# Performance work log

Measured on AMD Instinct MI355X. Metric: run time of the kernel, lower is better.

Reference implementation:

```python
import jax, jax.numpy as jnp
import numpy as np

N_NODES = 100000
N_EDGES = 3200000
NFEAT, H1, H2, NCLASS = 512, 300, 200, 40


def setup_inputs() -> dict:
    key = jax.random.key(0)
    ks = jax.random.split(key, 8)
    x = jax.random.normal(ks[0], (N_NODES, NFEAT), dtype=jnp.float32)
    edge_index = jax.random.randint(ks[1], (2, N_EDGES), 0, N_NODES, dtype=jnp.int32)
    edge_weight = jax.random.uniform(ks[2], (N_EDGES,), dtype=jnp.float32)
    def glorot(k, fi, fo):
        s = 1.0 / np.sqrt(fi)
        return jax.random.uniform(k, (fi, fo), jnp.float32, -s, s)
    w1 = glorot(ks[3], NFEAT, H1)
    w2 = glorot(ks[4], H1, H2)
    w3 = glorot(ks[5], H2, NCLASS)
    return {
        'x': x, 'edge_index': edge_index, 'edge_weight': edge_weight,
        'w1': w1, 'b1': jnp.zeros((H1,), jnp.float32),
        'w2': w2, 'b2': jnp.zeros((H2,), jnp.float32),
        'w3': w3, 'b3': jnp.zeros((NCLASS,), jnp.float32),
    }


def _gcn_layer(h, edge_index, edge_weight, w, b):
    # support = h @ W ; out = A @ support + b  (A given as weighted edge list)
    support = h @ w                                   # [N, out]
    src, dst = edge_index[0], edge_index[1]
    msgs = support[src] * edge_weight[:, None]        # gather + scale, [E, out]
    agg = jax.ops.segment_sum(msgs, dst, num_segments=h.shape[0])
    return agg + b


def reference(x, edge_index, edge_weight, w1, b1, w2, b2, w3, b3):
    h1 = jax.nn.relu(_gcn_layer(x, edge_index, edge_weight, w1, b1))
    h2 = jax.nn.relu(_gcn_layer(h1, edge_index, edge_weight, w2, b2))
    logits = _gcn_layer(h2, edge_index, edge_weight, w3, b3)
    return jax.nn.softmax(logits, axis=1)
```

## Files before the change

### kernel.cpp

```cpp
#include <hip/hip_runtime.h>
#include <hip/hip_bf16.h>
#include <hip/hip_fp16.h>
#include <math.h>

#define NFEAT 512
#define H1 300
#define H2 200
#define NCLASS 40

typedef __attribute__((ext_vector_type(8))) _Float16 half8;
typedef __attribute__((ext_vector_type(4))) float f32x4;
typedef __attribute__((ext_vector_type(2))) unsigned int u32x2;

__device__ __forceinline__ void stage16(const void* gptr, void* ldsptr) {
    __builtin_amdgcn_global_load_lds(
        (const __attribute__((address_space(1))) unsigned int*)gptr,
        (__attribute__((address_space(3))) unsigned int*)ldsptr,
        16, 0, 0);
}

__device__ __forceinline__ unsigned short f2h(float f) {
    return __half_as_ushort(__float2half(f));
}
__device__ __forceinline__ float h2f(unsigned short u) {
    return __half2float(__ushort_as_half(u));
}
__device__ __forceinline__ float2 h2f2(unsigned int u) {
    __half2 h = *reinterpret_cast<__half2*>(&u);
    return __half22float2(h);
}
__device__ __forceinline__ unsigned pack2h(float a, float b) {
    return (unsigned)f2h(a) | ((unsigned)f2h(b) << 16);
}


__global__ __launch_bounds__(256) void count_dst_kernel(const int* __restrict__ dst,
                                                        int* __restrict__ counts, int E) {
    int i = blockIdx.x * blockDim.x + threadIdx.x;
    if (i < E) atomicAdd(&counts[dst[i]], 1);
}

__global__ __launch_bounds__(1024) void scan_kernel(const int* __restrict__ counts,
                                                    int* __restrict__ row_ptr,
                                                    int* __restrict__ nextp, int N) {
    __shared__ int sums[1024];
    const int tid = threadIdx.x;
    const int CH = (N + 1023) >> 10;
    const int b = tid * CH;
    const int e = min(b + CH, N);
    int s = 0;
    for (int i = b; i < e; i++) s += counts[i];
    sums[tid] = s;
    __syncthreads();
    #pragma unroll
    for (int off = 1; off < 1024; off <<= 1) {
        int t = (tid >= off) ? sums[tid - off] : 0;
        __syncthreads();
        sums[tid] += t;
        __syncthreads();
    }
    int run = (tid > 0) ? sums[tid - 1] : 0;
    for (int i = b; i < e; i++) {
        row_ptr[i] = run;
        nextp[i] = run;
        run += counts[i];
    }
    if (tid == 0) row_ptr[N] = sums[1023];
}

__global__ __launch_bounds__(256) void fill_csr_kernel(const int* __restrict__ src,
                                                       const int* __restrict__ dst,
                                                       const float* __restrict__ ew,
                                                       int* __restrict__ next,
                                                       int2* __restrict__ csr_sw, int E) {
    int i = blockIdx.x * blockDim.x + threadIdx.x;
    if (i < E) {
        int d = dst[i];
        int pos = atomicAdd(&next[d], 1);
        csr_sw[pos] = make_int2(src[i], __float_as_int(ew[i]));
    }
}


__global__ __launch_bounds__(256) void convert_x_kernel(const float* __restrict__ x,
                                                        unsigned short* __restrict__ X16,
                                                        int total8) {
    int stride = gridDim.x * 256;
    for (int i = blockIdx.x * 256 + threadIdx.x; i < total8; i += stride) {
        const float* p = x + (size_t)i * 8;
        float4 a = *(const float4*)p;
        float4 b = *(const float4*)(p + 4);
        half8 h;
        h[0] = (_Float16)a.x; h[1] = (_Float16)a.y;
        h[2] = (_Float16)a.z; h[3] = (_Float16)a.w;
        h[4] = (_Float16)b.x; h[5] = (_Float16)b.y;
        h[6] = (_Float16)b.z; h[7] = (_Float16)b.w;
        *(half8*)(X16 + (size_t)i * 8) = h;
    }
}


__global__ __launch_bounds__(256) void split_weights_kernel(
        const float* __restrict__ w1, const float* __restrict__ w2, const float* __restrict__ w3,
        unsigned short* __restrict__ W1H, unsigned short* __restrict__ W1L,
        unsigned short* __restrict__ W2H, unsigned short* __restrict__ W2L,
        unsigned short* __restrict__ W3H, unsigned short* __restrict__ W3L) {
    int i = blockIdx.x * 256 + threadIdx.x;
    const float* w; unsigned short *H, *L; int K, N, KP;
    if (i < 163840) {
        w = w1; H = W1H; L = W1L; K = 512; N = 300; KP = 512;
    } else if (i < 163840 + 81920) {
        i -= 163840; w = w2; H = W2H; L = W2L; K = 300; N = 200; KP = 320;
    } else {
        i -= 245760; w = w3; H = W3H; L = W3L; K = 200; N = 40; KP = 256;
    }
    int n = i / KP, k = i - n * KP;
    float a = (n < N && k < K) ? w[(size_t)k * N + n] : 0.f;
    unsigned short h = f2h(a);
    H[i] = h;
    L[i] = f2h(a - h2f(h));
}


template <int KPAD, int NT, bool AF32>
__global__ __launch_bounds__(256, 3) void gemm_f16_kernel(
        const void* __restrict__ A_,
        const unsigned short* __restrict__ Bhi, const unsigned short* __restrict__ Blo,
        unsigned short* __restrict__ C, int M, int NP, int MT) {
    __shared__ short Bs_hi[4096];
    __shared__ short Bs_lo[4096];

    const int id = blockIdx.x;
    const int g  = id / (8 * NT);
    const int r  = id % (8 * NT);
    const int nt = r >> 3;
    const int x  = r & 7;
    const int mt = g * 8 + x;
    if (mt >= MT) return;

    const int tid = threadIdx.x;
    const int wave = tid >> 6, lane = tid & 63;
    const int lm = lane & 15, quad = lane >> 4;
    const int bm = mt * 256, bn = nt * 64;

    f32x4 acc[4][4] = {};

    for (int k0 = 0; k0 < KPAD; k0 += 64) {
        #pragma unroll
        for (int i = 0; i < 2; i++) {
            int t = i * 256 + tid;
            int n = t >> 3;
            int c = (t & 7) ^ (n & 7);
            size_t goff = (size_t)(bn + n) * KPAD + (size_t)(k0 + c * 8);
            int lbase = (i * 256 + wave * 64) * 8;
            stage16(Bhi + goff, Bs_hi + lbase);
            stage16(Blo + goff, Bs_lo + lbase);
        }
        __syncthreads();

        #pragma unroll
        for (int h = 0; h < 2; h++) {
            const int cidx = h * 4 + quad;
            half8 a[4], bh[4], bl[4];
            #pragma unroll
            for (int i = 0; i < 4; i++) {
                int row = bm + wave * 64 + i * 16 + lm;
                row = row < M ? row : M - 1;
                size_t off = (size_t)row * KPAD + (size_t)(k0 + cidx * 8);
                if (AF32) {
                    const float* ap = (const float*)A_ + off;
                    float4 p = *(const float4*)ap;
                    float4 q = *(const float4*)(ap + 4);
                    half8 t8;
                    t8[0] = (_Float16)p.x; t8[1] = (_Float16)p.y;
                    t8[2] = (_Float16)p.z; t8[3] = (_Float16)p.w;
                    t8[4] = (_Float16)q.x; t8[5] = (_Float16)q.y;
                    t8[6] = (_Float16)q.z; t8[7] = (_Float16)q.w;
                    a[i] = t8;
                } else {
                    a[i] = *(const half8*)((const unsigned short*)A_ + off);
                }
            }
            #pragma unroll
            for (int j = 0; j < 4; j++) {
                int n = j * 16 + lm;
                int off = (n * 8 + (cidx ^ (n & 7))) * 8;
                bh[j] = *(const half8*)(Bs_hi + off);
                bl[j] = *(const half8*)(Bs_lo + off);
            }
            #pragma unroll
            for (int i = 0; i < 4; i++)
                #pragma unroll
                for (int j = 0; j < 4; j++) {
                    acc[i][j] = __builtin_amdgcn_mfma_f32_16x16x32_f16(a[i], bh[j], acc[i][j], 0, 0, 0);
                    acc[i][j] = __builtin_amdgcn_mfma_f32_16x16x32_f16(a[i], bl[j], acc[i][j], 0, 0, 0);
                }
        }
        __syncthreads();
    }

    #pragma unroll
    for (int i = 0; i < 4; i++) {
        #pragma unroll
        for (int j = 0; j < 4; j++) {
            #pragma unroll
            for (int r2 = 0; r2 < 4; r2++) {
                int row = bm + wave * 64 + i * 16 + quad * 4 + r2;
                int col = bn + j * 16 + lm;
                if (row < M && col < NP)
                    C[(size_t)row * NP + col] = f2h(acc[i][j][r2]);
            }
        }
    }
}


template <int F, int NPS, int NPO>
__global__ __launch_bounds__(256) void spmm_relu_f16_kernel(
        const int* __restrict__ row_ptr, const int2* __restrict__ csr_sw,
        const unsigned short* __restrict__ support, const float* __restrict__ bias,
        unsigned short* __restrict__ outp, int N) {
    constexpr int F4 = F / 4;
    constexpr int NP4 = NPO / 4;
    constexpr int NCH = (F4 + 63) / 64;
    constexpr int NCHW = (NP4 + 63) / 64;

    int row = blockIdx.x * 4 + (threadIdx.x >> 6);
    int lane = threadIdx.x & 63;
    if (row >= N) return;
    int beg = row_ptr[row], end = row_ptr[row + 1];

    float acc[NCHW][4] = {};

    int e = beg;
    int nb8 = (end - beg) >> 3;
    if (nb8 > 0) {
        int2 swbuf[8];
        #pragma unroll
        for (int q = 0; q < 8; q++) swbuf[q] = csr_sw[e + q];
        for (int b = 0; b < nb8; b++) {
            int s_[8]; float w_[8];
            #pragma unroll
            for (int q = 0; q < 8; q++) {
                s_[q] = __builtin_amdgcn_readfirstlane(swbuf[q].x);
                w_[q] = __uint_as_float((unsigned)__builtin_amdgcn_readfirstlane(swbuf[q].y));
            }
            u32x2 u[8][NCH];
            #pragma unroll
            for (int q = 0; q < 8; q++) {
                const unsigned short* sp = support + (size_t)s_[q] * NPS;
                #pragma unroll
                for (int j = 0; j < NCH; j++) {
                    int f4 = j * 64 + lane;
                    if (f4 < F4) u[q][j] = *(const u32x2*)(sp + f4 * 4);
                }
            }
            int enext = e + 8;
            if (b + 1 < nb8) {
                #pragma unroll
                for (int q = 0; q < 8; q++) swbuf[q] = csr_sw[enext + q];
            }
            #pragma unroll
            for (int q = 0; q < 8; q++) {
                #pragma unroll
                for (int j = 0; j < NCH; j++) {
                    int f4 = j * 64 + lane;
                    if (f4 < F4) {
                        float2 a0 = h2f2(u[q][j].x), a1 = h2f2(u[q][j].y);
                        acc[j][0] += w_[q] * a0.x;
                        acc[j][1] += w_[q] * a0.y;
                        acc[j][2] += w_[q] * a1.x;
                        acc[j][3] += w_[q] * a1.y;
                    }
                }
            }
            e = enext;
        }
    }
    for (; e + 3 < end; e += 4) {
        int s_[4]; float w_[4];
        #pragma unroll
        for (int q = 0; q < 4; q++) {
            int2 sw = csr_sw[e + q];
            s_[q] = __builtin_amdgcn_readfirstlane(sw.x);
            w_[q] = __uint_as_float((unsigned)__builtin_amdgcn_readfirstlane(sw.y));
        }
        u32x2 u[4][NCH];
        #pragma unroll
        for (int q = 0; q < 4; q++) {
            const unsigned short* sp = support + (size_t)s_[q] * NPS;
            #pragma unroll
            for (int j = 0; j < NCH; j++) {
                int f4 = j * 64 + lane;
                if (f4 < F4) u[q][j] = *(const u32x2*)(sp + f4 * 4);
            }
        }
        #pragma unroll
        for (int q = 0; q < 4; q++) {
            #pragma unroll
            for (int j = 0; j < NCH; j++) {
                int f4 = j * 64 + lane;
                if (f4 < F4) {
                    float2 a0 = h2f2(u[q][j].x), a1 = h2f2(u[q][j].y);
                    acc[j][0] += w_[q] * a0.x;
                    acc[j][1] += w_[q] * a0.y;
                    acc[j][2] += w_[q] * a1.x;
                    acc[j][3] += w_[q] * a1.y;
                }
            }
        }
    }
    for (; e < end; e++) {
        int2 sw = csr_sw[e];
        int ssrc = __builtin_amdgcn_readfirstlane(sw.x);
        float w0 = __uint_as_float((unsigned)__builtin_amdgcn_readfirstlane(sw.y));
        const unsigned short* sp = support + (size_t)ssrc * NPS;
        #pragma unroll
        for (int j = 0; j < NCH; j++) {
            int f4 = j * 64 + lane;
            if (f4 < F4) {
                u32x2 u = *(const u32x2*)(sp + f4 * 4);
                float2 a0 = h2f2(u.x), a1 = h2f2(u.y);
                acc[j][0] += w0 * a0.x;
                acc[j][1] += w0 * a0.y;
                acc[j][2] += w0 * a1.x;
                acc[j][3] += w0 * a1.y;
            }
        }
    }

    #pragma unroll
    for (int j = 0; j < NCHW; j++) {
        int f4 = j * 64 + lane;
        if (f4 < NP4) {
            bool real = f4 < F4;
            float4 bb = real ? ((const float4*)bias)[f4] : make_float4(0, 0, 0, 0);
            float v0 = real ? fmaxf(acc[j][0] + bb.x, 0.f) : 0.f;
            float v1 = real ? fmaxf(acc[j][1] + bb.y, 0.f) : 0.f;
            float v2 = real ? fmaxf(acc[j][2] + bb.z, 0.f) : 0.f;
            float v3 = real ? fmaxf(acc[j][3] + bb.w, 0.f) : 0.f;
            u32x2 w;
            w.x = pack2h(v0, v1);
            w.y = pack2h(v2, v3);
            *(u32x2*)(outp + (size_t)row * NPO + f4 * 4) = w;
        }
    }
}


__global__ __launch_bounds__(256) void spmm_softmax_kernel(
        const int* __restrict__ row_ptr, const int2* __restrict__ csr_sw,
        const unsigned short* __restrict__ support, const float* __restrict__ bias,
        float* __restrict__ out, int N) {
    int row = blockIdx.x * 4 + (threadIdx.x >> 6);
    int lane = threadIdx.x & 63;
    if (row >= N) return;
    int beg = row_ptr[row], end = row_ptr[row + 1];

    const int g = lane / 20;
    const int t = lane - g * 20;
    const bool lact = lane < 60;

    float a0 = 0.f, a1 = 0.f;
    for (int e = beg; e < end; e += 3) {
        int ei = e + g;
        bool v = lact && (ei < end);
        int2 sw = csr_sw[v ? ei : beg];
        float w = v ? __int_as_float(sw.y) : 0.f;
        unsigned u = *(const unsigned*)(support + (size_t)sw.x * 40 + t * 2);
        float2 aa = h2f2(u);
        a0 += w * aa.x;
        a1 += w * aa.y;
    }
    a0 += __shfl(a0, lane + 20) + __shfl(a0, lane + 40);
    a1 += __shfl(a1, lane + 20) + __shfl(a1, lane + 40);

    const bool act = lane < 20;
    float v0 = 0.f, v1 = 0.f, m = -INFINITY;
    if (act) {
        float2 bb = ((const float2*)bias)[t];
        v0 = a0 + bb.x;
        v1 = a1 + bb.y;
        m = fmaxf(v0, v1);
    }
    #pragma unroll
    for (int off = 16; off; off >>= 1) m = fmaxf(m, __shfl_xor(m, off));
    float e0 = 0.f, e1 = 0.f;
    if (act) { e0 = expf(v0 - m); e1 = expf(v1 - m); }
    float s = e0 + e1;
    #pragma unroll
    for (int off = 16; off; off >>= 1) s += __shfl_xor(s, off);
    if (act) {
        float inv = 1.f / s;
        *(float2*)(out + (size_t)row * NCLASS + t * 2) = make_float2(e0 * inv, e1 * inv);
    }
}


extern "C" void kernel_launch(void* const* d_in, const int* in_sizes, int n_in,
                              void* d_out, int out_size, void* d_ws, size_t ws_size,
                              hipStream_t stream) {
    const float* x   = (const float*)d_in[0];
    const int*   ei  = (const int*)d_in[1];
    const float* ew  = (const float*)d_in[2];
    const float* w1  = (const float*)d_in[3];
    const float* b1  = (const float*)d_in[4];
    const float* w2  = (const float*)d_in[5];
    const float* b2  = (const float*)d_in[6];
    const float* w3  = (const float*)d_in[7];
    const float* b3  = (const float*)d_in[8];
    float* out = (float*)d_out;

    const int N = in_sizes[0] / NFEAT;
    const int E = in_sizes[2];
    const int* src = ei;
    const int* dst = ei + E;

    const int KP1 = 512, NP1 = 320, NT1 = 5;
    const int KP2 = 320, NP2 = 200, NT2 = 4;
    const int KP3 = 256, NP3 = 40,  NT3 = 1;

    char* base = (char*)d_ws;
    unsigned short* X16 = (unsigned short*)(base);
    unsigned short* H1H = (unsigned short*)(base);
    unsigned short* H2H = (unsigned short*)(base);

    unsigned short* support = (unsigned short*)(base + 102400256);

    size_t wo = 102400256 + 64000256;
    auto walloc = [&](size_t bytes) { void* r = base + wo; wo += (bytes + 255) & ~(size_t)255; return r; };
    unsigned short* W1H = (unsigned short*)walloc((size_t)320 * 512 * 2);
    unsigned short* W1L = (unsigned short*)walloc((size_t)320 * 512 * 2);
    unsigned short* W2H = (unsigned short*)walloc((size_t)256 * 320 * 2);
    unsigned short* W2L = (unsigned short*)walloc((size_t)256 * 320 * 2);
    unsigned short* W3H = (unsigned short*)walloc((size_t)64 * 256 * 2);
    unsigned short* W3L = (unsigned short*)walloc((size_t)64 * 256 * 2);
    int*  counts  = (int*)walloc((size_t)N * 4);
    int*  row_ptr = (int*)walloc((size_t)(N + 1) * 4);
    int*  nextp   = (int*)walloc((size_t)N * 4);
    int2* csr_sw  = (int2*)walloc((size_t)E * 8);

    const int MT = (N + 255) / 256;
    const int G  = (MT + 7) / 8;
    const int wgs = (N + 3) / 4;
    const int EB = (E + 255) / 256;

    hipMemsetAsync(counts, 0, (size_t)N * 4, stream);
    count_dst_kernel<<<EB, 256, 0, stream>>>(dst, counts, E);
    scan_kernel<<<1, 1024, 0, stream>>>(counts, row_ptr, nextp, N);
    fill_csr_kernel<<<EB, 256, 0, stream>>>(src, dst, ew, nextp, csr_sw, E);

    split_weights_kernel<<<1024, 256, 0, stream>>>(w1, w2, w3, W1H, W1L, W2H, W2L, W3H, W3L);
    convert_x_kernel<<<2048, 256, 0, stream>>>(x, X16, N * NFEAT / 8);

    gemm_f16_kernel<KP1, NT1, false><<<G * 8 * NT1, 256, 0, stream>>>(
        X16, W1H, W1L, support, N, NP1, MT);
    spmm_relu_f16_kernel<H1, 320, 320><<<wgs, 256, 0, stream>>>(row_ptr, csr_sw, support, b1, H1H, N);

    gemm_f16_kernel<KP2, NT2, false><<<G * 8 * NT2, 256, 0, stream>>>(
        H1H, W2H, W2L, support, N, NP2, MT);
    spmm_relu_f16_kernel<H2, 200, 256><<<wgs, 256, 0, stream>>>(row_ptr, csr_sw, support, b2, H2H, N);

    gemm_f16_kernel<KP3, NT3, false><<<G * 8 * NT3, 256, 0, stream>>>(
        H2H, W3H, W3L, support, N, NP3, MT);
    spmm_softmax_kernel<<<wgs, 256, 0, stream>>>(row_ptr, csr_sw, support, b3, out, N);
}
```

Measured before the change: 1.665 ms.

## Fuse x fp32-to-fp16 conversion into first GEMM and split CSR fill into passes

Removes the separate convert_x kernel and has the first GEMM read fp32 x directly through its `true` template path, which saves a full write and re-read of the fp16 copy. The CSR fill is split into 8 passes over destination ranges so each pass's scattered atomics and writes hit a smaller region and stay cache-resident. The cost is that the edge list is read 8 times, and the first GEMM may load fp32 less efficiently.

```diff
diff --git a/kernel.cpp b/kernel.cpp
--- a/kernel.cpp
+++ b/kernel.cpp
@@ -68,34 +68,20 @@
     if (tid == 0) row_ptr[N] = sums[1023];
 }
 
-__global__ __launch_bounds__(256) void fill_csr_kernel(const int* __restrict__ src,
-                                                       const int* __restrict__ dst,
-                                                       const float* __restrict__ ew,
-                                                       int* __restrict__ next,
-                                                       int2* __restrict__ csr_sw, int E) {
+
+__global__ __launch_bounds__(256) void fill_csr_pass_kernel(const int* __restrict__ src,
+                                                            const int* __restrict__ dst,
+                                                            const float* __restrict__ ew,
+                                                            int* __restrict__ next,
+                                                            int2* __restrict__ csr_sw,
+                                                            int E, int lo, int hi) {
     int i = blockIdx.x * blockDim.x + threadIdx.x;
     if (i < E) {
         int d = dst[i];
-        int pos = atomicAdd(&next[d], 1);
-        csr_sw[pos] = make_int2(src[i], __float_as_int(ew[i]));
-    }
-}
-
-
-__global__ __launch_bounds__(256) void convert_x_kernel(const float* __restrict__ x,
-                                                        unsigned short* __restrict__ X16,
-                                                        int total8) {
-    int stride = gridDim.x * 256;
-    for (int i = blockIdx.x * 256 + threadIdx.x; i < total8; i += stride) {
-        const float* p = x + (size_t)i * 8;
-        float4 a = *(const float4*)p;
-        float4 b = *(const float4*)(p + 4);
-        half8 h;
-        h[0] = (_Float16)a.x; h[1] = (_Float16)a.y;
-        h[2] = (_Float16)a.z; h[3] = (_Float16)a.w;
-        h[4] = (_Float16)b.x; h[5] = (_Float16)b.y;
-        h[6] = (_Float16)b.z; h[7] = (_Float16)b.w;
-        *(half8*)(X16 + (size_t)i * 8) = h;
+        if (d >= lo && d < hi) {
+            int pos = atomicAdd(&next[d], 1);
+            csr_sw[pos] = make_int2(src[i], __float_as_int(ew[i]));
+        }
     }
 }
 
@@ -421,7 +407,6 @@
     const int KP3 = 256, NP3 = 40,  NT3 = 1;
 
     char* base = (char*)d_ws;
-    unsigned short* X16 = (unsigned short*)(base);
     unsigned short* H1H = (unsigned short*)(base);
     unsigned short* H2H = (unsigned short*)(base);
 
@@ -448,13 +433,20 @@
     hipMemsetAsync(counts, 0, (size_t)N * 4, stream);
     count_dst_kernel<<<EB, 256, 0, stream>>>(dst, counts, E);
     scan_kernel<<<1, 1024, 0, stream>>>(counts, row_ptr, nextp, N);
-    fill_csr_kernel<<<EB, 256, 0, stream>>>(src, dst, ew, nextp, csr_sw, E);
+    {
+        const int P = 8;
+        const int CHN = (N + P - 1) / P;
+        for (int p = 0; p < P; p++) {
+            int lo = p * CHN;
+            int hi = min(N, lo + CHN);
+            fill_csr_pass_kernel<<<EB, 256, 0, stream>>>(src, dst, ew, nextp, csr_sw, E, lo, hi);
+        }
+    }
 
     split_weights_kernel<<<1024, 256, 0, stream>>>(w1, w2, w3, W1H, W1L, W2H, W2L, W3H, W3L);
-    convert_x_kernel<<<2048, 256, 0, stream>>>(x, X16, N * NFEAT / 8);
-
-    gemm_f16_kernel<KP1, NT1, false><<<G * 8 * NT1, 256, 0, stream>>>(
-        X16, W1H, W1L, support, N, NP1, MT);
+
+    gemm_f16_kernel<KP1, NT1, true><<<G * 8 * NT1, 256, 0, stream>>>(
+        x, W1H, W1L, support, N, NP1, MT);
     spmm_relu_f16_kernel<H1, 320, 320><<<wgs, 256, 0, stream>>>(row_ptr, csr_sw, support, b1, H1H, N);
 
     gemm_f16_kernel<KP2, NT2, false><<<G * 8 * NT2, 256, 0, stream>>>(
```

Result: faster. 1.625 ms (-2.5%).
